# Performance work log

Hardware: AMD Instinct MI355X
Metric: run time of the kernel (lower is better)

## Reference

```python
import jax, jax.numpy as jnp
import numpy as np

B, T, D, U = 64, 512, 512, 1024
LN_EPS = 1e-3  # keras LayerNormalization default


def setup_inputs() -> dict:
    key = jax.random.key(0)
    ks = jax.random.split(key, 6)
    s = 0.02
    return {
        "x": jax.random.normal(ks[0], (B, T, D), jnp.float32),
        "W1": jax.random.normal(ks[1], (D, 4 * U), jnp.float32) * s,
        "R1": jax.random.normal(ks[2], (U, 4 * U), jnp.float32) * s,
        "b1": jnp.zeros((4 * U,), jnp.float32),
        "gamma1": jnp.ones((U,), jnp.float32),
        "beta1": jnp.zeros((U,), jnp.float32),
        "W2": jax.random.normal(ks[3], (U, 4 * U), jnp.float32) * s,
        "R2": jax.random.normal(ks[4], (U, 4 * U), jnp.float32) * s,
        "b2": jnp.zeros((4 * U,), jnp.float32),
        "gamma2": jnp.ones((U,), jnp.float32),
        "beta2": jnp.zeros((U,), jnp.float32),
    }


def lstm_linear(x_btd, W, R, b, return_sequences):
    """Keras LSTM with activation=None: i,f,o sigmoid gates, identity candidate/output."""
    units = R.shape[0]
    # Precompute input projection for all timesteps: [B,T,4U]
    zx = jnp.einsum('btd,dk->btk', x_btd, W) + b

    def step(carry, zx_t):
        h, c = carry
        z = zx_t + h @ R  # [B,4U]
        zi, zf, zg, zo = jnp.split(z, 4, axis=-1)
        i = jax.nn.sigmoid(zi)
        f = jax.nn.sigmoid(zf)
        o = jax.nn.sigmoid(zo)
        c = f * c + i * zg          # activation=None -> linear candidate
        h = o * c                   # activation=None -> linear output
        return (h, c), h

    bsz = x_btd.shape[0]
    init = (jnp.zeros((bsz, units), x_btd.dtype), jnp.zeros((bsz, units), x_btd.dtype))
    (h_last, _), hs = jax.lax.scan(step, init, jnp.swapaxes(zx, 0, 1))  # hs: [T,B,U]
    return jnp.swapaxes(hs, 0, 1) if return_sequences else h_last


def layernorm(x, gamma, beta, eps=LN_EPS):
    mu = jnp.mean(x, axis=-1, keepdims=True)
    var = jnp.mean(jnp.square(x - mu), axis=-1, keepdims=True)
    return (x - mu) * jax.lax.rsqrt(var + eps) * gamma + beta


def reference(x, W1, R1, b1, gamma1, beta1, W2, R2, b2, gamma2, beta2):
    # Layer 1: LSTM (return_sequences=True) -> LayerNorm -> tanh
    h = lstm_linear(x, W1, R1, b1, return_sequences=True)   # [B,T,U]
    h = jnp.tanh(layernorm(h, gamma1, beta1))
    # Layer 2: LSTM (return_sequences=False) -> LayerNorm -> tanh
    h = lstm_linear(h, W2, R2, b2, return_sequences=False)  # [B,U]
    h = jnp.tanh(layernorm(h, gamma2, beta2))
    return h
```

## Files before the change

kernel.cpp:

```cpp
#include <hip/hip_runtime.h>
#include <stdint.h>

#define B_ 64
#define T_ 512
#define D_ 512
#define U_ 1024
#define TC 32
#define NCH 16

typedef unsigned short u16;
typedef unsigned long long u64;
typedef u16 ushort8  __attribute__((ext_vector_type(8)));
typedef __bf16 bf16x8 __attribute__((ext_vector_type(8)));
typedef float f32x4  __attribute__((ext_vector_type(4)));

static __device__ __forceinline__ u16 f2bf(float f) {
  unsigned u = __builtin_bit_cast(unsigned, f);
  u += 0x7FFFu + ((u >> 16) & 1u);
  return (u16)(u >> 16);
}
static __device__ __forceinline__ float bf2f(u16 h) {
  unsigned u = ((unsigned)h) << 16;
  return __builtin_bit_cast(float, u);
}


__global__ __launch_bounds__(256) void pack_wt(const float* __restrict__ src,
                                               u16* __restrict__ dst, int K) {
  __shared__ float tile[32][33];
  int n0 = blockIdx.x * 32, k0 = blockIdx.y * 32;
  int tx = threadIdx.x, ty = threadIdx.y;
#pragma unroll
  for (int r = 0; r < 4; ++r) {
    int k = k0 + ty + r * 8;
    tile[ty + r * 8][tx] = src[(long)k * 4096 + n0 + tx];
  }
  __syncthreads();
#pragma unroll
  for (int r = 0; r < 4; ++r) {
    int n = n0 + ty + r * 8;
    int np = ((n & 1023) << 2) | (n >> 10);
    dst[(long)np * K + k0 + tx] = f2bf(tile[tx][ty + r * 8]);
  }
}

__global__ __launch_bounds__(256) void pack_bias(const float* __restrict__ b1,
                                                 const float* __restrict__ b2,
                                                 float* __restrict__ bp) {
  int n = blockIdx.x * 256 + threadIdx.x;
  int np = ((n & 1023) << 2) | (n >> 10);
  bp[np] = b1[n];
  bp[4096 + np] = b2[n];
}


template <bool AF32>
__global__ __launch_bounds__(512) void zx_gemm(const void* __restrict__ Av, long sB, long sT,
                                               int K, const u16* __restrict__ Bp,
                                               const float* __restrict__ biasp,
                                               float* __restrict__ zxo) {
  __shared__ __align__(16) u16 Als[128][72];
  __shared__ __align__(16) u16 Bls[128][72];
  const int tid = threadIdx.x;
  const int mt = blockIdx.x, nt = blockIdx.y;
  const int l = tid & 63, w = tid >> 6;
  const int wm = w >> 2, wn = w & 3;
  const int sr = tid >> 2, skq = (tid & 3) * 16;

  const int gr = mt * 128 + sr;
  const int b = gr >> 5, tt = gr & 31;
  const long abase = (long)b * sB + (long)tt * sT;
  const float* Af = (const float*)Av;
  const u16* Ah = (const u16*)Av;

  const int nc = K >> 6;
  float4 raf[4];
  ushort8 rah[2];
  ushort8 rb[2];

  auto gload = [&](int ch) {
    long k0 = (long)ch << 6;
    if constexpr (AF32) {
#pragma unroll
      for (int i = 0; i < 4; ++i)
        raf[i] = *reinterpret_cast<const float4*>(Af + abase + k0 + skq + i * 4);
    } else {
#pragma unroll
      for (int i = 0; i < 2; ++i)
        rah[i] = *reinterpret_cast<const ushort8*>(Ah + abase + k0 + skq + i * 8);
    }
#pragma unroll
    for (int i = 0; i < 2; ++i)
      rb[i] = *reinterpret_cast<const ushort8*>(Bp + (long)(nt * 128 + sr) * K + k0 + skq + i * 8);
  };

  f32x4 acc[4][2];
#pragma unroll
  for (int fm = 0; fm < 4; ++fm)
#pragma unroll
    for (int fn = 0; fn < 2; ++fn) acc[fm][fn] = (f32x4){0.f, 0.f, 0.f, 0.f};

  gload(0);
  for (int ch = 0; ch < nc; ++ch) {
    __syncthreads();
    if constexpr (AF32) {
      const float* pr = (const float*)raf;
      ushort8 lo, hi;
#pragma unroll
      for (int j = 0; j < 8; ++j) { lo[j] = f2bf(pr[j]); hi[j] = f2bf(pr[8 + j]); }
      *reinterpret_cast<ushort8*>(&Als[sr][skq]) = lo;
      *reinterpret_cast<ushort8*>(&Als[sr][skq + 8]) = hi;
    } else {
      *reinterpret_cast<ushort8*>(&Als[sr][skq]) = rah[0];
      *reinterpret_cast<ushort8*>(&Als[sr][skq + 8]) = rah[1];
    }
    *reinterpret_cast<ushort8*>(&Bls[sr][skq]) = rb[0];
    *reinterpret_cast<ushort8*>(&Bls[sr][skq + 8]) = rb[1];
    __syncthreads();
    if (ch + 1 < nc) gload(ch + 1);
#pragma unroll
    for (int ks = 0; ks < 2; ++ks) {
#pragma unroll
      for (int fm = 0; fm < 4; ++fm) {
        bf16x8 a = __builtin_bit_cast(bf16x8,
            *reinterpret_cast<const ushort8*>(&Als[wm * 64 + fm * 16 + (l & 15)][ks * 32 + (l >> 4) * 8]));
#pragma unroll
        for (int fn = 0; fn < 2; ++fn) {
          bf16x8 bb = __builtin_bit_cast(bf16x8,
              *reinterpret_cast<const ushort8*>(&Bls[wn * 32 + fn * 16 + (l & 15)][ks * 32 + (l >> 4) * 8]));
          acc[fm][fn] = __builtin_amdgcn_mfma_f32_16x16x32_bf16(a, bb, acc[fm][fn], 0, 0, 0);
        }
      }
    }
  }

#pragma unroll
  for (int fm = 0; fm < 4; ++fm)
#pragma unroll
    for (int fn = 0; fn < 2; ++fn) {
      int col = nt * 128 + wn * 32 + fn * 16 + (l & 15);
      float bv = biasp[col];
#pragma unroll
      for (int j = 0; j < 4; ++j) {
        int row = mt * 128 + wm * 64 + fm * 16 + (l >> 4) * 4 + j;
        zxo[(long)row * 4096 + col] = acc[fm][fn][j] + bv;
      }
    }
}


__global__ __launch_bounds__(512) void lstm_chunk(
    const float* __restrict__ zx1, const u16* __restrict__ R1p, float* __restrict__ c1v,
    u16* __restrict__ h1_0, u16* __restrict__ h1_1, u16* __restrict__ h1s,
    const float* __restrict__ zx2, const u16* __restrict__ R2p, float* __restrict__ c2v,
    u16* __restrict__ h2_0, u16* __restrict__ h2_1,
    unsigned* __restrict__ flag1, unsigned* __restrict__ flag2,
    int g01, int g02, int act1, int act2) {
  const int layer = blockIdx.x >> 7;
  if (layer ? (!act2) : (!act1)) return;

  __shared__ __align__(16) u16 Als[16][1032];
  __shared__ __align__(16) u16 Bls[2][128][136];
  __shared__ float Zls[16][132];

  const float* zx = layer ? zx2 : zx1;
  const u16* Rp   = layer ? R2p : R1p;
  float* cv       = layer ? c2v : c1v;
  u16* hb0        = layer ? h2_0 : h1_0;
  u16* hb1        = layer ? h2_1 : h1_1;
  unsigned* flag  = layer ? flag2 : flag1;
  const int g0    = layer ? g02 : g01;

  const int lb = blockIdx.x & 127;
  const int q = lb >> 5;
  const int cg = lb & 31;
  const int n0 = cg * 128;
  const int u0 = cg * 32;

  const int tid = threadIdx.x;
  const int l = tid & 63, w = tid >> 6;

  const int tArow = tid >> 5, tAoff = (tid & 31) * 32;
  const int tBrow = tid >> 2, tBoff = (tid & 3) * 32;
  const int tgb = tid >> 5, tgun = tid & 31;
  const int bq = q * 16 + tgb;
  const int ug = u0 + tgun;

  float creg = cv[(long)bq * U_ + ug];

  ushort8 rbv[4];
  auto gloadB = [&](int ch) {
#pragma unroll
    for (int i = 0; i < 4; ++i)
      rbv[i] = *reinterpret_cast<const ushort8*>(Rp + (long)(n0 + tBrow) * U_ + ch * 128 + tBoff + i * 8);
  };

  for (int tt = 0; tt < TC; ++tt) {
    const int g = g0 + tt;

    if (g > 0) {
      if (tid == 0) {
        while (__hip_atomic_load(&flag[g - 1], __ATOMIC_RELAXED, __HIP_MEMORY_SCOPE_AGENT) < 128u)
          __builtin_amdgcn_s_sleep(2);
      }
      __syncthreads();
    }

    const u16* hr = (g & 1) ? hb0 : hb1;
    u16* hw       = (g & 1) ? hb1 : hb0;
    {
      u64* src = (u64*)(hr + (long)(q * 16 + tArow) * U_ + tAoff);
#pragma unroll
      for (int i = 0; i < 8; ++i) {
        u64 v = __hip_atomic_load(src + i, __ATOMIC_RELAXED, __HIP_MEMORY_SCOPE_AGENT);
        *reinterpret_cast<u64*>(&Als[tArow][tAoff + i * 4]) = v;
      }
    }

    f32x4 acc = {0.f, 0.f, 0.f, 0.f};
    gloadB(0);
#pragma unroll
    for (int i = 0; i < 4; ++i)
      *reinterpret_cast<ushort8*>(&Bls[0][tBrow][tBoff + i * 8]) = rbv[i];
    for (int ch = 0; ch < 8; ++ch) {
      if (ch < 7) gloadB(ch + 1);
      __syncthreads();
      if (ch < 7) {
#pragma unroll
        for (int i = 0; i < 4; ++i)
          *reinterpret_cast<ushort8*>(&Bls[(ch + 1) & 1][tBrow][tBoff + i * 8]) = rbv[i];
      }
#pragma unroll
      for (int ks = 0; ks < 4; ++ks) {
        bf16x8 a = __builtin_bit_cast(bf16x8,
            *reinterpret_cast<const ushort8*>(&Als[l & 15][ch * 128 + ks * 32 + (l >> 4) * 8]));
        bf16x8 bb = __builtin_bit_cast(bf16x8,
            *reinterpret_cast<const ushort8*>(&Bls[ch & 1][w * 16 + (l & 15)][ks * 32 + (l >> 4) * 8]));
        acc = __builtin_amdgcn_mfma_f32_16x16x32_bf16(a, bb, acc, 0, 0, 0);
      }
    }

    {
      int r0 = (l >> 4) * 4, col = w * 16 + (l & 15);
#pragma unroll
      for (int j = 0; j < 4; ++j) Zls[r0 + j][col] = acc[j];
    }
    __syncthreads();

    {
      f32x4 zr = *reinterpret_cast<const f32x4*>(&Zls[tgb][tgun * 4]);
      f32x4 zv = *reinterpret_cast<const f32x4*>(zx + ((long)bq * TC + tt) * 4096 + n0 + tgun * 4);
      float zi = zr[0] + zv[0], zf = zr[1] + zv[1], zg = zr[2] + zv[2], zo = zr[3] + zv[3];
      float ig = 1.f / (1.f + expf(-zi));
      float fg = 1.f / (1.f + expf(-zf));
      float og = 1.f / (1.f + expf(-zo));
      creg = fg * creg + ig * zg;
      u16 hv = f2bf(og * creg);
      unsigned hvn = __shfl_down((unsigned)hv, 1, 64);
      if ((tgun & 1) == 0) {
        unsigned pv = (unsigned)hv | (hvn << 16);
        __hip_atomic_store((unsigned*)(hw + (long)bq * U_ + ug), pv,
                           __ATOMIC_RELAXED, __HIP_MEMORY_SCOPE_AGENT);
      }
      if (layer == 0) h1s[((long)bq * T_ + g) * U_ + ug] = hv;
    }

    asm volatile("s_waitcnt vmcnt(0)" ::: "memory");
    __syncthreads();
    if (tid == 0)
      __hip_atomic_fetch_add(&flag[g], 1u, __ATOMIC_RELAXED, __HIP_MEMORY_SCOPE_AGENT);
  }

  cv[(long)bq * U_ + ug] = creg;
}


__global__ __launch_bounds__(256) void ln_chunk(const u16* __restrict__ h1seq, int t0,
                                                const float* __restrict__ gamma,
                                                const float* __restrict__ beta,
                                                u16* __restrict__ dst) {
  __shared__ float sbuf[8];
  int row = blockIdx.x;
  int b = row >> 5, tt = row & 31;
  const u16* src = h1seq + ((long)b * T_ + t0 + tt) * U_;
  u16* drow = dst + (long)row * U_;
  float x[4];
#pragma unroll
  for (int j = 0; j < 4; ++j) x[j] = bf2f(src[threadIdx.x + 256 * j]);
  float s = x[0] + x[1] + x[2] + x[3];
  for (int o = 32; o > 0; o >>= 1) s += __shfl_down(s, o, 64);
  if ((threadIdx.x & 63) == 0) sbuf[threadIdx.x >> 6] = s;
  __syncthreads();
  float mu = (sbuf[0] + sbuf[1] + sbuf[2] + sbuf[3]) * (1.f / 1024.f);
  float d[4], s2 = 0.f;
#pragma unroll
  for (int j = 0; j < 4; ++j) { d[j] = x[j] - mu; s2 += d[j] * d[j]; }
  for (int o = 32; o > 0; o >>= 1) s2 += __shfl_down(s2, o, 64);
  if ((threadIdx.x & 63) == 0) sbuf[4 + (threadIdx.x >> 6)] = s2;
  __syncthreads();
  float inv = rsqrtf((sbuf[4] + sbuf[5] + sbuf[6] + sbuf[7]) * (1.f / 1024.f) + 1e-3f);
#pragma unroll
  for (int j = 0; j < 4; ++j) {
    int u = threadIdx.x + 256 * j;
    drow[u] = f2bf(tanhf(d[j] * inv * gamma[u] + beta[u]));
  }
}

__global__ __launch_bounds__(256) void ln_tanh_final(const u16* __restrict__ h2,
                                                     const float* __restrict__ gamma,
                                                     const float* __restrict__ beta,
                                                     float* __restrict__ out) {
  __shared__ float sbuf[8];
  const u16* row = h2 + (long)blockIdx.x * U_;
  float x[4];
#pragma unroll
  for (int j = 0; j < 4; ++j) x[j] = bf2f(row[threadIdx.x + 256 * j]);
  float s = x[0] + x[1] + x[2] + x[3];
  for (int o = 32; o > 0; o >>= 1) s += __shfl_down(s, o, 64);
  if ((threadIdx.x & 63) == 0) sbuf[threadIdx.x >> 6] = s;
  __syncthreads();
  float mu = (sbuf[0] + sbuf[1] + sbuf[2] + sbuf[3]) * (1.f / 1024.f);
  float d[4], s2 = 0.f;
#pragma unroll
  for (int j = 0; j < 4; ++j) { d[j] = x[j] - mu; s2 += d[j] * d[j]; }
  for (int o = 32; o > 0; o >>= 1) s2 += __shfl_down(s2, o, 64);
  if ((threadIdx.x & 63) == 0) sbuf[4 + (threadIdx.x >> 6)] = s2;
  __syncthreads();
  float inv = rsqrtf((sbuf[4] + sbuf[5] + sbuf[6] + sbuf[7]) * (1.f / 1024.f) + 1e-3f);
#pragma unroll
  for (int j = 0; j < 4; ++j) {
    int u = threadIdx.x + 256 * j;
    out[(long)blockIdx.x * U_ + u] = tanhf(d[j] * inv * gamma[u] + beta[u]);
  }
}


extern "C" void kernel_launch(void* const* d_in, const int* in_sizes, int n_in,
                              void* d_out, int out_size, void* d_ws, size_t ws_size,
                              hipStream_t stream) {
  const float* x      = (const float*)d_in[0];
  const float* W1     = (const float*)d_in[1];
  const float* R1     = (const float*)d_in[2];
  const float* b1     = (const float*)d_in[3];
  const float* gamma1 = (const float*)d_in[4];
  const float* beta1  = (const float*)d_in[5];
  const float* W2     = (const float*)d_in[6];
  const float* R2     = (const float*)d_in[7];
  const float* b2     = (const float*)d_in[8];
  const float* gamma2 = (const float*)d_in[9];
  const float* beta2  = (const float*)d_in[10];
  float* out = (float*)d_out;

  char* base = (char*)d_ws;
  size_t off = 0;
  auto alloc = [&](size_t bytes) -> void* {
    void* p = base + off;
    off += (bytes + 255) & ~(size_t)255;
    return p;
  };
  u16*      Wp1   = (u16*)alloc((size_t)4096 * D_ * 2);
  u16*      Rp1   = (u16*)alloc((size_t)4096 * U_ * 2);
  u16*      Wp2   = (u16*)alloc((size_t)4096 * U_ * 2);
  u16*      Rp2   = (u16*)alloc((size_t)4096 * U_ * 2);
  float*    biasp = (float*)alloc((size_t)2 * 4096 * 4);
  float*    zxA   = (float*)alloc((size_t)B_ * TC * 4096 * 4);
  float*    zxB   = (float*)alloc((size_t)B_ * TC * 4096 * 4);
  u16*      h1seq = (u16*)alloc((size_t)B_ * T_ * U_ * 2);
  u16*      h1ln  = (u16*)alloc((size_t)B_ * TC * U_ * 2);
  float*    c1    = (float*)alloc((size_t)B_ * U_ * 4);
  float*    c2    = (float*)alloc((size_t)B_ * U_ * 4);
  u16*      h1a   = (u16*)alloc((size_t)B_ * U_ * 2);
  u16*      h1b   = (u16*)alloc((size_t)B_ * U_ * 2);
  u16*      h2a   = (u16*)alloc((size_t)B_ * U_ * 2);
  u16*      h2b   = (u16*)alloc((size_t)B_ * U_ * 2);
  unsigned* flag1 = (unsigned*)alloc((size_t)T_ * 4);
  unsigned* flag2 = (unsigned*)alloc((size_t)T_ * 4);

  pack_wt<<<dim3(128, 16), dim3(32, 8), 0, stream>>>(W1, Wp1, D_);
  pack_wt<<<dim3(128, 32), dim3(32, 8), 0, stream>>>(R1, Rp1, U_);
  pack_wt<<<dim3(128, 32), dim3(32, 8), 0, stream>>>(W2, Wp2, U_);
  pack_wt<<<dim3(128, 32), dim3(32, 8), 0, stream>>>(R2, Rp2, U_);
  pack_bias<<<16, 256, 0, stream>>>(b1, b2, biasp);
  hipMemsetAsync(c1, 0, (size_t)B_ * U_ * 4, stream);
  hipMemsetAsync(c2, 0, (size_t)B_ * U_ * 4, stream);
  hipMemsetAsync(h1b, 0, (size_t)B_ * U_ * 2, stream);
  hipMemsetAsync(h2b, 0, (size_t)B_ * U_ * 2, stream);
  hipMemsetAsync(flag1, 0, (size_t)T_ * 4, stream);
  hipMemsetAsync(flag2, 0, (size_t)T_ * 4, stream);

  for (int p = 0; p <= NCH; ++p) {
    int act1 = (p < NCH), act2 = (p >= 1);
    if (act1)
      zx_gemm<true><<<dim3(16, 32), 512, 0, stream>>>(
          (const void*)(x + (long)p * TC * D_), (long)T_ * D_, (long)D_, D_, Wp1, biasp, zxA);
    if (act2) {
      ln_chunk<<<B_ * TC, 256, 0, stream>>>(h1seq, (p - 1) * TC, gamma1, beta1, h1ln);
      zx_gemm<false><<<dim3(16, 32), 512, 0, stream>>>(
          (const void*)h1ln, (long)TC * U_, (long)U_, U_, Wp2, biasp + 4096, zxB);
    }
    const float* p_zx1 = zxA; const u16* p_R1 = Rp1; float* p_c1 = c1;
    u16* p_h10 = h1a; u16* p_h11 = h1b; u16* p_h1s = h1seq;
    const float* p_zx2 = zxB; const u16* p_R2 = Rp2; float* p_c2 = c2;
    u16* p_h20 = h2a; u16* p_h21 = h2b;
    unsigned* p_f1 = flag1; unsigned* p_f2 = flag2;
    int p_g01 = p * TC, p_g02 = (p - 1) * TC, p_a1 = act1, p_a2 = act2;
    void* args[17] = {&p_zx1, &p_R1, &p_c1, &p_h10, &p_h11, &p_h1s,
                      &p_zx2, &p_R2, &p_c2, &p_h20, &p_h21,
                      &p_f1, &p_f2, &p_g01, &p_g02, &p_a1, &p_a2};
    hipLaunchCooperativeKernel((void*)lstm_chunk, dim3(256), dim3(512), args, 0, stream);
  }
  ln_tanh_final<<<B_, 256, 0, stream>>>(h2b, gamma2, beta2, out);
}
```

Measured before the change: 6.276 ms.

## Keep recurrent weight slice resident in LDS and stream hidden state per step

Changes the recurrent LSTM kernel's work split. Each block now owns 8 units (32 gate columns) across all 64 batch rows, instead of 32 units across 16 batch rows. The block's 32x1024 slice of R is loaded into LDS once before the time loop, so it is no longer re-streamed from global memory every step. Each step instead loads the full 64x1024 hidden state into registers and stages it through LDS chunk by chunk. This removes repeated weight traffic, but adds more barriers per step and heavy register use (32 u64 values per thread).

Result: slower. 7.090 ms (+13.0%).

```diff
diff --git a/kernel.cpp b/kernel.cpp
--- a/kernel.cpp
+++ b/kernel.cpp
@@ -159,9 +159,9 @@
   const int layer = blockIdx.x >> 7;
   if (layer ? (!act2) : (!act1)) return;
 
-  __shared__ __align__(16) u16 Als[16][1032];
-  __shared__ __align__(16) u16 Bls[2][128][136];
-  __shared__ float Zls[16][132];
+  __shared__ __align__(16) u16 Rls[32][1032];
+  __shared__ __align__(16) u16 hb[64][136];
+  __shared__ float Zls[64][36];
 
   const float* zx = layer ? zx2 : zx1;
   const u16* Rp   = layer ? R2p : R1p;
@@ -171,85 +171,80 @@
   unsigned* flag  = layer ? flag2 : flag1;
   const int g0    = layer ? g02 : g01;
 
-  const int lb = blockIdx.x & 127;
-  const int q = lb >> 5;
-  const int cg = lb & 31;
-  const int n0 = cg * 128;
-  const int u0 = cg * 32;
+  const int cg = blockIdx.x & 127;
+  const int n0 = cg * 32;
+  const int u0 = cg * 8;
 
   const int tid = threadIdx.x;
   const int l = tid & 63, w = tid >> 6;
-
-  const int tArow = tid >> 5, tAoff = (tid & 31) * 32;
-  const int tBrow = tid >> 2, tBoff = (tid & 3) * 32;
-  const int tgb = tid >> 5, tgun = tid & 31;
-  const int bq = q * 16 + tgb;
-  const int ug = u0 + tgun;
-
-  float creg = cv[(long)bq * U_ + ug];
-
-  ushort8 rbv[4];
-  auto gloadB = [&](int ch) {
-#pragma unroll
-    for (int i = 0; i < 4; ++i)
-      rbv[i] = *reinterpret_cast<const ushort8*>(Rp + (long)(n0 + tBrow) * U_ + ch * 128 + tBoff + i * 8);
-  };
+  const int fm = w >> 1, fn = w & 1;
+
+  {
+    const int rr = tid >> 4, rk = (tid & 15) * 64;
+#pragma unroll
+    for (int i = 0; i < 8; ++i) {
+      ushort8 v = *reinterpret_cast<const ushort8*>(Rp + (long)(n0 + rr) * U_ + rk + i * 8);
+      *reinterpret_cast<ushort8*>(&Rls[rr][rk + i * 8]) = v;
+    }
+  }
+
+  const int tArow = tid >> 3, tAoff = (tid & 7) * 16;
+  const int guu = tid & 7;
+  float creg = cv[(long)tArow * U_ + u0 + guu];
+
+  __syncthreads();
 
   for (int tt = 0; tt < TC; ++tt) {
     const int g = g0 + tt;
 
-    if (g > 0) {
-      if (tid == 0) {
-        while (__hip_atomic_load(&flag[g - 1], __ATOMIC_RELAXED, __HIP_MEMORY_SCOPE_AGENT) < 128u)
-          __builtin_amdgcn_s_sleep(2);
+    if (g > 0 && tid == 0) {
+      while (__hip_atomic_load(&flag[g - 1], __ATOMIC_RELAXED, __HIP_MEMORY_SCOPE_AGENT) < 128u)
+        __builtin_amdgcn_s_sleep(2);
+    }
+    __syncthreads();
+
+    const u16* hr = (g & 1) ? hb0 : hb1;
+    u16* hw       = (g & 1) ? hb1 : hb0;
+
+    u64 rga[32];
+    {
+      const u64* src = (const u64*)(hr + (long)tArow * U_ + tAoff);
+#pragma unroll
+      for (int i = 0; i < 32; ++i)
+        rga[i] = __hip_atomic_load(src + (i >> 2) * 32 + (i & 3),
+                                   __ATOMIC_RELAXED, __HIP_MEMORY_SCOPE_AGENT);
+    }
+
+    f32x4 acc = {0.f, 0.f, 0.f, 0.f};
+#pragma unroll
+    for (int ch = 0; ch < 8; ++ch) {
+      __syncthreads();
+      {
+        u64* d = (u64*)&hb[tArow][tAoff];
+#pragma unroll
+        for (int j = 0; j < 4; ++j) d[j] = rga[ch * 4 + j];
       }
       __syncthreads();
-    }
-
-    const u16* hr = (g & 1) ? hb0 : hb1;
-    u16* hw       = (g & 1) ? hb1 : hb0;
-    {
-      u64* src = (u64*)(hr + (long)(q * 16 + tArow) * U_ + tAoff);
-#pragma unroll
-      for (int i = 0; i < 8; ++i) {
-        u64 v = __hip_atomic_load(src + i, __ATOMIC_RELAXED, __HIP_MEMORY_SCOPE_AGENT);
-        *reinterpret_cast<u64*>(&Als[tArow][tAoff + i * 4]) = v;
-      }
-    }
-
-    f32x4 acc = {0.f, 0.f, 0.f, 0.f};
-    gloadB(0);
-#pragma unroll
-    for (int i = 0; i < 4; ++i)
-      *reinterpret_cast<ushort8*>(&Bls[0][tBrow][tBoff + i * 8]) = rbv[i];
-    for (int ch = 0; ch < 8; ++ch) {
-      if (ch < 7) gloadB(ch + 1);
-      __syncthreads();
-      if (ch < 7) {
-#pragma unroll
-        for (int i = 0; i < 4; ++i)
-          *reinterpret_cast<ushort8*>(&Bls[(ch + 1) & 1][tBrow][tBoff + i * 8]) = rbv[i];
-      }
 #pragma unroll
       for (int ks = 0; ks < 4; ++ks) {
         bf16x8 a = __builtin_bit_cast(bf16x8,
-            *reinterpret_cast<const ushort8*>(&Als[l & 15][ch * 128 + ks * 32 + (l >> 4) * 8]));
+            *reinterpret_cast<const ushort8*>(&hb[fm * 16 + (l & 15)][ks * 32 + (l >> 4) * 8]));
         bf16x8 bb = __builtin_bit_cast(bf16x8,
-            *reinterpret_cast<const ushort8*>(&Bls[ch & 1][w * 16 + (l & 15)][ks * 32 + (l >> 4) * 8]));
+            *reinterpret_cast<const ushort8*>(&Rls[fn * 16 + (l & 15)][ch * 128 + ks * 32 + (l >> 4) * 8]));
         acc = __builtin_amdgcn_mfma_f32_16x16x32_bf16(a, bb, acc, 0, 0, 0);
       }
     }
 
     {
-      int r0 = (l >> 4) * 4, col = w * 16 + (l & 15);
-#pragma unroll
-      for (int j = 0; j < 4; ++j) Zls[r0 + j][col] = acc[j];
+      int r0 = (l >> 4) * 4, col = fn * 16 + (l & 15);
+#pragma unroll
+      for (int j = 0; j < 4; ++j) Zls[fm * 16 + r0 + j][col] = acc[j];
     }
     __syncthreads();
 
     {
-      f32x4 zr = *reinterpret_cast<const f32x4*>(&Zls[tgb][tgun * 4]);
-      f32x4 zv = *reinterpret_cast<const f32x4*>(zx + ((long)bq * TC + tt) * 4096 + n0 + tgun * 4);
+      f32x4 zr = *reinterpret_cast<const f32x4*>(&Zls[tArow][guu * 4]);
+      f32x4 zv = *reinterpret_cast<const f32x4*>(zx + ((long)tArow * TC + tt) * 4096 + n0 + guu * 4);
       float zi = zr[0] + zv[0], zf = zr[1] + zv[1], zg = zr[2] + zv[2], zo = zr[3] + zv[3];
       float ig = 1.f / (1.f + expf(-zi));
       float fg = 1.f / (1.f + expf(-zf));
@@ -257,12 +252,12 @@
       creg = fg * creg + ig * zg;
       u16 hv = f2bf(og * creg);
       unsigned hvn = __shfl_down((unsigned)hv, 1, 64);
-      if ((tgun & 1) == 0) {
+      if ((guu & 1) == 0) {
         unsigned pv = (unsigned)hv | (hvn << 16);
-        __hip_atomic_store((unsigned*)(hw + (long)bq * U_ + ug), pv,
+        __hip_atomic_store((unsigned*)(hw + (long)tArow * U_ + u0 + guu), pv,
                            __ATOMIC_RELAXED, __HIP_MEMORY_SCOPE_AGENT);
       }
-      if (layer == 0) h1s[((long)bq * T_ + g) * U_ + ug] = hv;
+      if (layer == 0) h1s[((long)tArow * T_ + g) * U_ + u0 + guu] = hv;
     }
 
     asm volatile("s_waitcnt vmcnt(0)" ::: "memory");
@@ -271,7 +266,7 @@
       __hip_atomic_fetch_add(&flag[g], 1u, __ATOMIC_RELAXED, __HIP_MEMORY_SCOPE_AGENT);
   }
 
-  cv[(long)bq * U_ + ug] = creg;
+  cv[(long)tArow * U_ + u0 + guu] = creg;
 }
 
 
```
